# Optimization experiments

Measured on AMD Instinct MI355X. Metric: run time of the kernel, lower is better.

Reference implementation:

```python
import jax, jax.numpy as jnp
import numpy as np

B, H, W, C = 8, 64, 64, 512
D = C // 8  # key/query/value projection dim per SAGAN block


def setup_inputs() -> dict:
    key = jax.random.key(0)
    ks = jax.random.split(key, 5)
    scale = 1.0 / np.sqrt(C)
    return {
        "x": jax.random.normal(ks[0], (B, H, W, C), dtype=jnp.float32),
        "Wf": jax.random.normal(ks[1], (C, D), dtype=jnp.float32) * scale,
        "bf": jnp.zeros((D,), dtype=jnp.float32),
        "Wg": jax.random.normal(ks[2], (C, D), dtype=jnp.float32) * scale,
        "bg": jnp.zeros((D,), dtype=jnp.float32),
        "Wh": jax.random.normal(ks[3], (C, D), dtype=jnp.float32) * scale,
        "bh": jnp.zeros((D,), dtype=jnp.float32),
        "Wv": jax.random.normal(ks[4], (D, C), dtype=jnp.float32) * (1.0 / np.sqrt(D)),
        "bv": jnp.zeros((C,), dtype=jnp.float32),
        "gamma": jnp.float32(0.01),
    }


def reference(x, Wf, bf, Wg, bg, Wh, bh, Wv, bv, gamma):
    b, h, w, c = x.shape
    n = h * w
    xf = x.reshape(b, n, c)  # flatten spatial dims: [B, N, C]
    # 1x1 convs == per-position dense projections
    f = xf @ Wf + bf  # [B, N, D]
    g = xf @ Wg + bg  # [B, N, D]
    hh = xf @ Wh + bh  # [B, N, D]
    # unscaled attention logits, softmax over keys (axis=-1)
    s = jnp.einsum("bnd,bmd->bnm", f, g)  # [B, N, N]
    attn = jax.nn.softmax(s, axis=-1)
    context = jnp.einsum("bnm,bmd->bnd", attn, hh)  # [B, N, D]
    # v conv (1x1) applied to gamma-scaled context, residual add
    o = (gamma * context) @ Wv + bv + xf  # [B, N, C]
    return o.reshape(b, h, w, c)
```

## Files before the change

### kernel.cpp

```cpp
#include <hip/hip_runtime.h>
#include <hip/hip_bf16.h>
#include <math.h>


typedef short v8s __attribute__((ext_vector_type(8)));
typedef unsigned short v4u __attribute__((ext_vector_type(4)));
typedef unsigned v4i __attribute__((ext_vector_type(4)));
typedef float v4f __attribute__((ext_vector_type(4)));

#define BB 8
#define NN 4096
#define CC 512
#define DD 64

__device__ __forceinline__ unsigned short f2bf(float f){
  union { float f; unsigned u; } v; v.f = f;
  unsigned r = (v.u + 0x7FFF + ((v.u >> 16) & 1)) >> 16;
  return (unsigned short)r;
}

#if __has_builtin(__builtin_amdgcn_cvt_pk_bf16_f32)
typedef __bf16 bf2_t __attribute__((ext_vector_type(2)));
__device__ __forceinline__ unsigned pkbf(float a, float b){
  bf2_t r = __builtin_amdgcn_cvt_pk_bf16_f32(a, b);
  union { bf2_t v; unsigned u; } c; c.v = r; return c.u;
}
#else
__device__ __forceinline__ unsigned pkbf(float a, float b){
  return (unsigned)f2bf(a) | ((unsigned)f2bf(b) << 16);
}
#endif

#if __has_builtin(__builtin_amdgcn_exp2f)
__device__ __forceinline__ float ex2(float x){ return __builtin_amdgcn_exp2f(x); }
#else
__device__ __forceinline__ float ex2(float x){ return exp2f(x); }
#endif

__device__ __forceinline__ void gload_lds16(const void* g, void* l){
  __builtin_amdgcn_global_load_lds(
      (const __attribute__((address_space(1))) void*)g,
      (__attribute__((address_space(3))) void*)l, 16, 0, 0);
}

__global__ void transpose_w(const float* __restrict__ Wf,
                            const float* __restrict__ Wg,
                            const float* __restrict__ Wh,
                            const float* __restrict__ Wv,
                            unsigned short* __restrict__ Wt,
                            unsigned short* __restrict__ Wvt){
  int idx = blockIdx.x * 256 + threadIdx.x;
  if (idx < 3 * DD * CC){
    int p = idx / (DD * CC); int rem = idx % (DD * CC);
    int d = rem / CC; int c = rem % CC;
    const float* W = (p == 0) ? Wf : ((p == 1) ? Wg : Wh);
    Wt[idx] = f2bf(W[c * DD + d]);
  } else {
    int idx2 = idx - 3 * DD * CC;
    if (idx2 < CC * DD){
      int c = idx2 / DD; int d = idx2 % DD;
      Wvt[idx2] = f2bf(Wv[d * CC + c]);
    }
  }
}

__global__ __launch_bounds__(512) void proj_kernel(
    const float* __restrict__ x,
    const unsigned short* __restrict__ Wt,
    const float* __restrict__ bf_,
    const float* __restrict__ bg_,
    const float* __restrict__ bh_,
    unsigned short* __restrict__ f,
    unsigned short* __restrict__ g,
    unsigned short* __restrict__ ht)
{
  __shared__ __align__(16) short lA[2][64][72];
  __shared__ __align__(16) short lB[2][192][72];
  int t = threadIdx.x;
  int w = t >> 6, lane = t & 63;
  int quad = lane >> 4, l16 = lane & 15;
  int rowbase = blockIdx.x * 64;
  int m0 = (w >> 1) * 16;
  int ch = w & 1;

  v4f acc[6];
  #pragma unroll
  for (int i = 0; i < 6; i++) acc[i] = (v4f){0.f, 0.f, 0.f, 0.f};

  int arow = t >> 3, aq8 = t & 7;
  const float* xrow = x + (rowbase + arow) * 512 + aq8 * 8;

  v4f a0, a1;
  v8s br[3];

  auto load_regs = [&](int kt){
    const float* xp = xrow + kt * 64;
    a0 = *(const v4f*)(xp);
    a1 = *(const v4f*)(xp + 4);
    #pragma unroll
    for (int r = 0; r < 3; r++){
      int chunk = t + r * 512;
      int row = chunk >> 3, c8 = chunk & 7;
      br[r] = *(const v8s*)(Wt + row * 512 + kt * 64 + c8 * 8);
    }
  };
  auto write_lds = [&](int buf){
    v4i c0 = { pkbf(a0[0],a0[1]), pkbf(a0[2],a0[3]),
               pkbf(a1[0],a1[1]), pkbf(a1[2],a1[3]) };
    *(v4i*)&lA[buf][arow][aq8 * 8] = c0;
    #pragma unroll
    for (int r = 0; r < 3; r++){
      int chunk = t + r * 512;
      int row = chunk >> 3, c8 = chunk & 7;
      *(v8s*)&lB[buf][row][c8 * 8] = br[r];
    }
  };

  load_regs(0);
  write_lds(0);
  __syncthreads();
  for (int kt = 0; kt < 8; ++kt){
    int cur = kt & 1;
    if (kt < 7) load_regs(kt + 1);
    v8s A0 = *(const v8s*)&lA[cur][m0 + l16][quad * 8];
    v8s A1 = *(const v8s*)&lA[cur][m0 + l16][quad * 8 + 32];
    #pragma unroll
    for (int cb = 0; cb < 6; ++cb){
      int cbg = ch * 6 + cb;
      v8s b0 = *(const v8s*)&lB[cur][cbg * 16 + l16][quad * 8];
      v8s b1 = *(const v8s*)&lB[cur][cbg * 16 + l16][quad * 8 + 32];
      acc[cb] = __builtin_amdgcn_mfma_f32_16x16x32_bf16(A0, b0, acc[cb], 0, 0, 0);
      acc[cb] = __builtin_amdgcn_mfma_f32_16x16x32_bf16(A1, b1, acc[cb], 0, 0, 0);
    }
    if (kt < 7) write_lds(cur ^ 1);
    __syncthreads();
  }

  #pragma unroll
  for (int cb = 0; cb < 6; ++cb){
    int cbg = ch * 6 + cb;
    if (cbg < 8){
      int col = cbg * 16 + l16;
      int p = col >> 6, d = col & 63;
      float bb = (p == 0) ? bf_[d] : bg_[d];
      #pragma unroll
      for (int r = 0; r < 4; r++){
        int gr = rowbase + m0 + quad * 4 + r;
        float val = acc[cb][r] + bb;
        if (p == 0) f[gr * 64 + d] = f2bf(val * 1.44269504f);
        else        g[gr * 64 + d] = f2bf(val);
      }
    }
  }

  short (*lT)[65] = (short(*)[65])lB;
  if (ch == 1){
    #pragma unroll
    for (int cb = 2; cb < 6; ++cb){
      int d = (cb - 2) * 16 + l16;
      float bb = bh_[d];
      #pragma unroll
      for (int r = 0; r < 4; r++)
        lT[m0 + quad * 4 + r][d] = (short)f2bf(acc[cb][r] + bb);
    }
  }
  __syncthreads();
  {
    int dd = t >> 3, nseg = t & 7;
    v8s h0;
    #pragma unroll
    for (int i = 0; i < 8; i++)
      h0[i] = lT[nseg * 8 + i][dd];
    int bidx = rowbase >> 12;
    int n0 = (rowbase & 4095) + nseg * 8;
    unsigned short* hp = ht + ((size_t)(bidx * 64 + dd)) * 4096 + n0;
    *(v8s*)hp = h0;
  }
}

__global__ __launch_bounds__(256) void flash_kernel(
    const unsigned short* __restrict__ f,
    const unsigned short* __restrict__ g,
    const unsigned short* __restrict__ ht,
    float* __restrict__ Opart,
    float* __restrict__ lipart,
    unsigned short* __restrict__ ctx,
    int niter, int direct)
{
  __shared__ __align__(16) short lK[2][64 * 64];
  __shared__ __align__(16) short lV[2][64 * 64];
  __shared__ __align__(16) short lP[4][8][16][8];
  int t = threadIdx.x;
  int w = t >> 6, lane = t & 63;
  int quad = lane >> 4, l16 = lane & 15;
  int qt = blockIdx.x, sp = blockIdx.y, b = blockIdx.z;
  int q0 = qt * 128;
  int m0 = w * 32;

  const unsigned short* fb = f  + b * NN * 64;
  const unsigned short* gb = g  + b * NN * 64;
  const unsigned short* hb = ht + b * 64 * NN;

  const unsigned short* qbase = fb + (q0 + m0 + l16) * 64;
  v8s QB00 = *(const v8s*)(qbase + quad * 8);
  v8s QB01 = *(const v8s*)(qbase + quad * 8 + 32);
  v8s QB10 = *(const v8s*)(qbase + 16 * 64 + quad * 8);
  v8s QB11 = *(const v8s*)(qbase + 16 * 64 + quad * 8 + 32);

  int j0 = sp * niter;
  const char* srcK[2]; const char* srcV[2];
  char* dstK[2][2]; char* dstV[2][2];
  #pragma unroll
  for (int k = 0; k < 2; k++){
    int row = w * 16 + k * 8 + (lane >> 3);
    int c = (lane & 7) ^ (row & 7);
    srcK[k] = (const char*)gb + (size_t)j0 * 8192 + row * 128 + c * 16;
    srcV[k] = (const char*)hb + (size_t)row * 8192 + (size_t)j0 * 128 + c * 16;
    #pragma unroll
    for (int b2 = 0; b2 < 2; b2++){
      dstK[b2][k] = (char*)lK[b2] + w * 2048 + k * 1024;
      dstV[b2][k] = (char*)lV[b2] + w * 2048 + k * 1024;
    }
  }

  int ph = quad ^ (l16 & 7);
  const short* kA0[2]; const short* kA1[2];
  const short* vB0[2]; const short* vB1[2];
  #pragma unroll
  for (int b2 = 0; b2 < 2; b2++){
    kA0[b2] = lK[b2] + l16 * 64 + ph * 8;
    kA1[b2] = lK[b2] + l16 * 64 + (ph ^ 4) * 8;
    vB0[b2] = lV[b2] + l16 * 64 + ph * 8;
    vB1[b2] = lV[b2] + l16 * 64 + (ph ^ 4) * 8;
  }

  v8s ones;
  #pragma unroll
  for (int i = 0; i < 8; i++) ones[i] = (short)0x3F80;

  v4f rz[2];
  rz[0] = (v4f){0.f, 0.f, 0.f, 0.f};
  rz[1] = (v4f){0.f, 0.f, 0.f, 0.f};
  v4f O[2][4];
  #pragma unroll
  for (int gi = 0; gi < 2; gi++)
    #pragma unroll
    for (int cb = 0; cb < 4; cb++) O[gi][cb] = (v4f){0.f, 0.f, 0.f, 0.f};

  auto stage = [&](int b2){
    #pragma unroll
    for (int k = 0; k < 2; k++){
      gload_lds16(srcK[k], dstK[b2][k]);
      gload_lds16(srcV[k], dstV[b2][k]);
      srcK[k] += 8192; srcV[k] += 128;
    }
  };

  auto compute = [&](int b2){
    v4f st[2][4];
    __builtin_amdgcn_s_setprio(1);
    #pragma unroll
    for (int cb = 0; cb < 4; cb++){
      v8s a0 = *(const v8s*)(kA0[b2] + cb * 1024);
      v8s a1 = *(const v8s*)(kA1[b2] + cb * 1024);
      v4f z0 = (v4f){0.f, 0.f, 0.f, 0.f};
      z0 = __builtin_amdgcn_mfma_f32_16x16x32_bf16(a0, QB00, z0, 0, 0, 0);
      st[0][cb] = __builtin_amdgcn_mfma_f32_16x16x32_bf16(a1, QB01, z0, 0, 0, 0);
      v4f z1 = (v4f){0.f, 0.f, 0.f, 0.f};
      z1 = __builtin_amdgcn_mfma_f32_16x16x32_bf16(a0, QB10, z1, 0, 0, 0);
      st[1][cb] = __builtin_amdgcn_mfma_f32_16x16x32_bf16(a1, QB11, z1, 0, 0, 0);
    }
    __builtin_amdgcn_s_setprio(0);

    auto packwrite = [&](int gi){
      #pragma unroll
      for (int cb = 0; cb < 4; cb++){
        float p0 = ex2(st[gi][cb][0]);
        float p1 = ex2(st[gi][cb][1]);
        float p2 = ex2(st[gi][cb][2]);
        float p3 = ex2(st[gi][cb][3]);
        unsigned d0 = __builtin_amdgcn_perm(__float_as_uint(p1), __float_as_uint(p0), 0x07060302u);
        unsigned d1 = __builtin_amdgcn_perm(__float_as_uint(p3), __float_as_uint(p2), 0x07060302u);
        uint2 pk; pk.x = d0; pk.y = d1;
        *(uint2*)&lP[w][cb * 2 + (quad >> 1)][l16][(quad & 1) * 4] = pk;
      }
    };

    packwrite(0);
    v8s PA00 = *(const v8s*)&lP[w][quad][l16][0];
    v8s PA01 = *(const v8s*)&lP[w][quad + 4][l16][0];
    packwrite(1);

    v8s vb[4][2];
    #pragma unroll
    for (int cb = 0; cb < 4; cb++){
      vb[cb][0] = *(const v8s*)(vB0[b2] + cb * 1024);
      vb[cb][1] = *(const v8s*)(vB1[b2] + cb * 1024);
    }

    __builtin_amdgcn_s_setprio(1);
    rz[0] = __builtin_amdgcn_mfma_f32_16x16x32_bf16(PA00, ones, rz[0], 0, 0, 0);
    rz[0] = __builtin_amdgcn_mfma_f32_16x16x32_bf16(PA01, ones, rz[0], 0, 0, 0);
    #pragma unroll
    for (int cb = 0; cb < 4; cb++){
      O[0][cb] = __builtin_amdgcn_mfma_f32_16x16x32_bf16(PA00, vb[cb][0], O[0][cb], 0, 0, 0);
      O[0][cb] = __builtin_amdgcn_mfma_f32_16x16x32_bf16(PA01, vb[cb][1], O[0][cb], 0, 0, 0);
    }
    __builtin_amdgcn_s_setprio(0);

    v8s PA10 = *(const v8s*)&lP[w][quad][l16][0];
    v8s PA11 = *(const v8s*)&lP[w][quad + 4][l16][0];

    __builtin_amdgcn_s_setprio(1);
    rz[1] = __builtin_amdgcn_mfma_f32_16x16x32_bf16(PA10, ones, rz[1], 0, 0, 0);
    rz[1] = __builtin_amdgcn_mfma_f32_16x16x32_bf16(PA11, ones, rz[1], 0, 0, 0);
    #pragma unroll
    for (int cb = 0; cb < 4; cb++){
      O[1][cb] = __builtin_amdgcn_mfma_f32_16x16x32_bf16(PA10, vb[cb][0], O[1][cb], 0, 0, 0);
      O[1][cb] = __builtin_amdgcn_mfma_f32_16x16x32_bf16(PA11, vb[cb][1], O[1][cb], 0, 0, 0);
    }
    __builtin_amdgcn_s_setprio(0);
  };

  stage(0);
  __syncthreads();
  for (int jj = 0; jj < niter; jj += 2){
    stage(1);
    compute(0);
    __syncthreads();
    if (jj + 2 < niter) stage(0);
    compute(1);
    __syncthreads();
  }

  if (direct){
    #pragma unroll
    for (int gi = 0; gi < 2; gi++){
      float inv[4];
      #pragma unroll
      for (int r = 0; r < 4; r++)
        inv[r] = 1.0f / rz[gi][r];
      #pragma unroll
      for (int cb = 0; cb < 4; cb++)
        #pragma unroll
        for (int r = 0; r < 4; r++){
          int row = q0 + m0 + gi * 16 + quad * 4 + r;
          ctx[(b * NN + row) * 64 + cb * 16 + l16] = f2bf(O[gi][cb][r] * inv[r]);
        }
    }
  } else {
    int bf = (b * 32 + qt) * 4 + sp;
    if (l16 == 0){
      #pragma unroll
      for (int gi = 0; gi < 2; gi++)
        #pragma unroll
        for (int r = 0; r < 4; r++)
          lipart[bf * 128 + m0 + gi * 16 + quad * 4 + r] = rz[gi][r];
    }
    float* Ob = Opart + (size_t)bf * 8192;
    #pragma unroll
    for (int gi = 0; gi < 2; gi++)
      #pragma unroll
      for (int cb = 0; cb < 4; cb++)
        #pragma unroll
        for (int r = 0; r < 4; r++)
          Ob[(m0 + gi * 16 + quad * 4 + r) * 64 + cb * 16 + l16] = O[gi][cb][r];
  }
}

__global__ __launch_bounds__(256) void reduce_kernel(
    const float* __restrict__ Opart,
    const float* __restrict__ lipart,
    unsigned short* __restrict__ ctx)
{
  int i4 = blockIdx.x * 256 + threadIdx.x;
  int bqt = i4 >> 11;
  int rem = (i4 & 2047) << 2;
  int rl  = rem >> 6;
  const float* Ob  = Opart  + (size_t)bqt * 4 * 8192;
  const float* lib = lipart + bqt * 4 * 128;
  v4f s = *(const v4f*)(Ob + rem);
  s = s + *(const v4f*)(Ob + 8192  + rem);
  s = s + *(const v4f*)(Ob + 16384 + rem);
  s = s + *(const v4f*)(Ob + 24576 + rem);
  float li = (lib[rl] + lib[128 + rl]) + (lib[256 + rl] + lib[384 + rl]);
  float inv = 1.0f / li;
  uint2 o; o.x = pkbf(s[0] * inv, s[1] * inv); o.y = pkbf(s[2] * inv, s[3] * inv);
  *(uint2*)(ctx + (size_t)bqt * 8192 + rem) = o;
}

__global__ __launch_bounds__(256) void outproj_kernel(
    const unsigned short* __restrict__ ctx,
    const unsigned short* __restrict__ Wvt,
    const float* __restrict__ bv,
    const float* __restrict__ x,
    const float* __restrict__ gamma_p,
    float* __restrict__ out)
{
  __shared__ __align__(16) short lA[64][72];
  __shared__ __align__(16) short lB[128][72];
  int t = threadIdx.x;
  int w = t >> 6, lane = t & 63;
  int quad = lane >> 4, l16 = lane & 15;
  int rowbase = blockIdx.x * 64;
  int colbase = blockIdx.y * 128;
  float gamma = *gamma_p;

  #pragma unroll
  for (int r = 0; r < 2; r++){
    int chunk = t + r * 256;
    int row = chunk >> 3, c8 = chunk & 7;
    *(v8s*)&lA[row][c8 * 8] = *(const v8s*)(ctx + (rowbase + row) * 64 + c8 * 8);
  }
  #pragma unroll
  for (int r = 0; r < 4; r++){
    int chunk = t + r * 256;
    int row = chunk >> 3, c8 = chunk & 7;
    *(v8s*)&lB[row][c8 * 8] = *(const v8s*)(Wvt + (colbase + row) * 64 + c8 * 8);
  }
  __syncthreads();
  int m0 = w * 16;
  v8s A0 = *(const v8s*)&lA[m0 + l16][quad * 8];
  v8s A1 = *(const v8s*)&lA[m0 + l16][quad * 8 + 32];
  v4f acc[8];
  #pragma unroll
  for (int cb = 0; cb < 8; cb++){
    v8s b0 = *(const v8s*)&lB[cb * 16 + l16][quad * 8];
    v8s b1 = *(const v8s*)&lB[cb * 16 + l16][quad * 8 + 32];
    v4f z = (v4f){0.f, 0.f, 0.f, 0.f};
    z = __builtin_amdgcn_mfma_f32_16x16x32_bf16(A0, b0, z, 0, 0, 0);
    acc[cb] = __builtin_amdgcn_mfma_f32_16x16x32_bf16(A1, b1, z, 0, 0, 0);
  }
  #pragma unroll
  for (int cb = 0; cb < 8; cb++){
    int col = colbase + cb * 16 + l16;
    float bvv = bv[col];
    #pragma unroll
    for (int r = 0; r < 4; r++){
      int gr = rowbase + m0 + quad * 4 + r;
      out[gr * 512 + col] = gamma * acc[cb][r] + bvv + x[gr * 512 + col];
    }
  }
}

extern "C" void kernel_launch(void* const* d_in, const int* in_sizes, int n_in,
                              void* d_out, int out_size, void* d_ws, size_t ws_size,
                              hipStream_t stream) {
  const float* x   = (const float*)d_in[0];
  const float* Wf  = (const float*)d_in[1];
  const float* bf_ = (const float*)d_in[2];
  const float* Wg  = (const float*)d_in[3];
  const float* bg  = (const float*)d_in[4];
  const float* Wh  = (const float*)d_in[5];
  const float* bh  = (const float*)d_in[6];
  const float* Wv  = (const float*)d_in[7];
  const float* bv  = (const float*)d_in[8];
  const float* gam = (const float*)d_in[9];
  float* out = (float*)d_out;

  char* ws = (char*)d_ws;
  unsigned short* Wt  = (unsigned short*)(ws);
  unsigned short* Wvt = (unsigned short*)(ws + 196608);
  unsigned short* f   = (unsigned short*)(ws + 262144);
  unsigned short* g   = (unsigned short*)(ws + 4456448);
  unsigned short* ht  = (unsigned short*)(ws + 8650752);
  unsigned short* ctx = (unsigned short*)(ws + 12845056);
  float* Opart  = (float*)(ws + 17039360);
  float* lipart = (float*)(ws + 50593792);

  transpose_w<<<512, 256, 0, stream>>>(Wf, Wg, Wh, Wv, Wt, Wvt);
  proj_kernel<<<512, 512, 0, stream>>>(x, Wt, bf_, bg, bh, f, g, ht);

  bool split = (ws_size >= (size_t)51118080);
  if (split){
    flash_kernel<<<dim3(32, 4, 8), 256, 0, stream>>>(f, g, ht, Opart, lipart, ctx, 16, 0);
    reduce_kernel<<<2048, 256, 0, stream>>>(Opart, lipart, ctx);
  } else {
    flash_kernel<<<dim3(32, 1, 8), 256, 0, stream>>>(f, g, ht, nullptr, nullptr, ctx, 64, 1);
  }
  outproj_kernel<<<dim3(512, 4), 256, 0, stream>>>(ctx, Wvt, bv, x, gam, out);
}
```

Measured before the change: 214.9 us.

## Fuse split-K reduction with output projection into one kernel

Replaces the separate reduce kernel and output-projection kernel with one kernel. It sums the four flash partials, normalizes them, and writes the bf16 context tile into LDS. It then multiplies that tile by the full Wv (512 columns, XOR-swizzled in LDS) with MFMA and applies gamma, bias and the residual. This removes one launch and the ctx round trip through global memory. In exchange each block loads all of Wv, and the output stores are strided per lane (column-contiguous across l16 only).

```diff
diff --git a/kernel.cpp b/kernel.cpp
--- a/kernel.cpp
+++ b/kernel.cpp
@@ -368,25 +368,79 @@
   }
 }
 
-__global__ __launch_bounds__(256) void reduce_kernel(
+__global__ __launch_bounds__(512) void outfuse_kernel(
     const float* __restrict__ Opart,
     const float* __restrict__ lipart,
-    unsigned short* __restrict__ ctx)
+    const unsigned short* __restrict__ Wvt,
+    const float* __restrict__ bv,
+    const float* __restrict__ x,
+    const float* __restrict__ gamma_p,
+    float* __restrict__ out)
 {
-  int i4 = blockIdx.x * 256 + threadIdx.x;
-  int bqt = i4 >> 11;
-  int rem = (i4 & 2047) << 2;
-  int rl  = rem >> 6;
-  const float* Ob  = Opart  + (size_t)bqt * 4 * 8192;
-  const float* lib = lipart + bqt * 4 * 128;
-  v4f s = *(const v4f*)(Ob + rem);
-  s = s + *(const v4f*)(Ob + 8192  + rem);
-  s = s + *(const v4f*)(Ob + 16384 + rem);
-  s = s + *(const v4f*)(Ob + 24576 + rem);
-  float li = (lib[rl] + lib[128 + rl]) + (lib[256 + rl] + lib[384 + rl]);
-  float inv = 1.0f / li;
-  uint2 o; o.x = pkbf(s[0] * inv, s[1] * inv); o.y = pkbf(s[2] * inv, s[3] * inv);
-  *(uint2*)(ctx + (size_t)bqt * 8192 + rem) = o;
+  __shared__ __align__(16) short lA[64][72];
+  __shared__ __align__(16) short lB[512][64];
+  int t = threadIdx.x;
+  int lane = t & 63;
+  int w = t >> 6;
+  int quad = lane >> 4, l16 = lane & 15;
+  int rowbase = blockIdx.x * 64;
+  float gamma = *gamma_p;
+
+  {
+    int rl = t >> 3, d8 = (t & 7) * 8;
+    int group = rowbase >> 7;
+    int inrow = (rowbase & 127) + rl;
+    const float* Ob  = Opart  + (size_t)group * 32768 + inrow * 64 + d8;
+    const float* lib = lipart + group * 512 + inrow;
+    v4f s0 = *(const v4f*)(Ob);
+    v4f s1 = *(const v4f*)(Ob + 4);
+    float li = lib[0];
+    #pragma unroll
+    for (int sp = 1; sp < 4; sp++){
+      s0 = s0 + *(const v4f*)(Ob + sp * 8192);
+      s1 = s1 + *(const v4f*)(Ob + sp * 8192 + 4);
+      li += lib[sp * 128];
+    }
+    float inv = 1.0f / li;
+    v4i c = { pkbf(s0[0]*inv, s0[1]*inv), pkbf(s0[2]*inv, s0[3]*inv),
+              pkbf(s1[0]*inv, s1[1]*inv), pkbf(s1[2]*inv, s1[3]*inv) };
+    *(v4i*)&lA[rl][d8] = c;
+  }
+  #pragma unroll
+  for (int r = 0; r < 8; r++){
+    int chunk = t + r * 512;
+    int row = chunk >> 3, c8 = chunk & 7;
+    *(v8s*)&lB[row][(c8 ^ (row & 7)) * 8] =
+        *(const v8s*)(Wvt + row * 64 + c8 * 8);
+  }
+  __syncthreads();
+
+  int m0 = (w & 3) * 16;
+  int colhalf = w >> 2;
+  v8s A0 = *(const v8s*)&lA[m0 + l16][quad * 8];
+  v8s A1 = *(const v8s*)&lA[m0 + l16][quad * 8 + 32];
+  int ph = quad ^ (l16 & 7);
+  v4f acc[16];
+  #pragma unroll
+  for (int cb = 0; cb < 16; cb++){
+    int row = (colhalf * 16 + cb) * 16 + l16;
+    const short* bp = &lB[row][0];
+    v8s b0 = *(const v8s*)(bp + ph * 8);
+    v8s b1 = *(const v8s*)(bp + (ph ^ 4) * 8);
+    v4f z = (v4f){0.f, 0.f, 0.f, 0.f};
+    z = __builtin_amdgcn_mfma_f32_16x16x32_bf16(A0, b0, z, 0, 0, 0);
+    acc[cb] = __builtin_amdgcn_mfma_f32_16x16x32_bf16(A1, b1, z, 0, 0, 0);
+  }
+  #pragma unroll
+  for (int cb = 0; cb < 16; cb++){
+    int col = colhalf * 256 + cb * 16 + l16;
+    float bvv = bv[col];
+    #pragma unroll
+    for (int r = 0; r < 4; r++){
+      int gr = rowbase + m0 + quad * 4 + r;
+      out[gr * 512 + col] = gamma * acc[cb][r] + bvv + x[gr * 512 + col];
+    }
+  }
 }
 
 __global__ __launch_bounds__(256) void outproj_kernel(
@@ -474,9 +528,9 @@
   bool split = (ws_size >= (size_t)51118080);
   if (split){
     flash_kernel<<<dim3(32, 4, 8), 256, 0, stream>>>(f, g, ht, Opart, lipart, ctx, 16, 0);
-    reduce_kernel<<<2048, 256, 0, stream>>>(Opart, lipart, ctx);
+    outfuse_kernel<<<512, 512, 0, stream>>>(Opart, lipart, Wvt, bv, x, gam, out);
   } else {
     flash_kernel<<<dim3(32, 1, 8), 256, 0, stream>>>(f, g, ht, nullptr, nullptr, ctx, 64, 1);
-  }
-  outproj_kernel<<<dim3(512, 4), 256, 0, stream>>>(ctx, Wvt, bv, x, gam, out);
-}
+    outproj_kernel<<<dim3(512, 4), 256, 0, stream>>>(ctx, Wvt, bv, x, gam, out);
+  }
+}
```

Measured after the change: 202.7 us. 5.7% less time.
